# Performance work log

Measured on AMD Instinct MI355X. Metric: run time of the kernel, lower is better.

The kernel has to match this reference:

```python
import jax, jax.numpy as jnp
import numpy as np

NHEAD = 16

def setup_inputs() -> dict:
    key = jax.random.key(0)
    ks = jax.random.split(key, 7)
    b, l, d = 4, 2048, 1024
    s = 1.0 / np.sqrt(d)
    return {
        "Q": jax.random.normal(ks[0], (b, l, d), jnp.float32),
        "K": jax.random.normal(ks[1], (b, l, d), jnp.float32),
        "V": jax.random.normal(ks[2], (b, l, d), jnp.float32),
        "WQ": jax.random.normal(ks[3], (d, d), jnp.float32) * s,
        "WK": jax.random.normal(ks[4], (d, d), jnp.float32) * s,
        "WV": jax.random.normal(ks[5], (d, d), jnp.float32) * s,
        "WO": jax.random.normal(ks[6], (d, d), jnp.float32) * s,
    }

def reference(Q, K, V, WQ, WK, WV, WO):
    # WQ/WK/WV/WO stored torch-style as [out, in]; Linear(x) = x @ W.T
    b, lq, d = Q.shape
    lk = K.shape[1]
    h = NHEAD
    dk = d // h
    # project and split heads: [b, l, h, dk]
    q = (Q @ WQ.T).reshape(b, lq, h, dk)
    k = (K @ WK.T).reshape(b, lk, h, dk)
    v = (V @ WV.T).reshape(b, lk, h, dk)
    # scaled dot-product attention (dropout = identity in eval mode)
    scale = 1.0 / jnp.sqrt(jnp.asarray(dk, Q.dtype))
    score = jnp.einsum('bqhd,bkhd->bhqk', q, k) * scale  # [b,h,lq,lk]
    attn = jax.nn.softmax(score, axis=-1)
    o = jnp.einsum('bhqk,bkhd->bqhd', attn, v).reshape(b, lq, h * dk)
    return o @ WO.T
```

## Files before the change

kernel.cpp:

```cpp
#include <hip/hip_runtime.h>
#include <stdint.h>

#define D_MODEL 1024
#define NHEADS 16
#define DKH 64
#define SEQ 2048
#define BATCH 4
#define M_TOT (BATCH * SEQ)
#define LOG2E 1.44269504088896340736f

typedef __bf16 v8bf __attribute__((ext_vector_type(8)));
typedef __bf16 v4bf __attribute__((ext_vector_type(4)));
typedef _Float16 v4h __attribute__((ext_vector_type(4)));
typedef float v4f __attribute__((ext_vector_type(4)));

typedef const __attribute__((address_space(1))) void* gas_ptr;
typedef __attribute__((address_space(3))) void* las_ptr;

static __device__ __forceinline__ void async16(const void* g, void* l) {
    __builtin_amdgcn_global_load_lds((gas_ptr)g, (las_ptr)l, 16, 0, 0);
}

static __device__ __forceinline__ v4f mfma16x32(v8bf a, v8bf b, v4f c) {
    return __builtin_amdgcn_mfma_f32_16x16x32_bf16(a, b, c, 0, 0, 0);
}
static __device__ __forceinline__ v4f mfma16x16h(v4h a, v4h b, v4f c) {
    return __builtin_amdgcn_mfma_f32_16x16x16f16(a, b, c, 0, 0, 0);
}

__global__ __launch_bounds__(256) void cvt_w(const float* __restrict__ w0,
                                             const float* __restrict__ w1,
                                             const float* __restrict__ w2,
                                             const float* __restrict__ w3,
                                             __bf16* __restrict__ dst) {
    int gid = blockIdx.x * 256 + threadIdx.x;
    int tsel = gid >> 17;
    int off = gid & 131071;
    const float* s = (tsel == 0) ? w0 : (tsel == 1) ? w1 : (tsel == 2) ? w2 : w3;
    const float4* sp = (const float4*)s + 2 * (size_t)off;
    float4 a = sp[0], b = sp[1];
    v8bf o;
    o[0] = (__bf16)a.x; o[1] = (__bf16)a.y; o[2] = (__bf16)a.z; o[3] = (__bf16)a.w;
    o[4] = (__bf16)b.x; o[5] = (__bf16)b.y; o[6] = (__bf16)b.z; o[7] = (__bf16)b.w;
    *(v8bf*)(dst + ((size_t)tsel << 20) + (size_t)off * 8) = o;
}

__global__ __launch_bounds__(256) void gemm_qkv(const float* __restrict__ Q,
                                                const float* __restrict__ K,
                                                const float* __restrict__ V,
                                                const __bf16* __restrict__ Wb,
                                                __bf16* __restrict__ qh,
                                                __bf16* __restrict__ kh,
                                                _Float16* __restrict__ vt) {
    const int t = threadIdx.x, lane = t & 63, wave = t >> 6;
    const int r = lane & 15, qd = lane >> 4;
    const int z = blockIdx.z;
    const int m0 = blockIdx.x * 128, n0 = blockIdx.y * 128;
    const int mw = (wave & 1) * 64, nw = (wave >> 1) * 64;
    const float* A = (z == 0) ? Q : (z == 1) ? K : V;
    const __bf16* W = Wb + ((size_t)z << 20);

    __shared__ __align__(16) __bf16 As[128 * 32];
    __shared__ __align__(16) __bf16 Bs[128 * 32];

    const int arow = t >> 1, ak = (t & 1) * 16;
    const float* ag = A + (size_t)(m0 + arow) * D_MODEL + ak;
    const int aswz = (arow >> 1) & 3;
    const int p0 = ((t & 1) * 2) ^ aswz, p1 = ((t & 1) * 2 + 1) ^ aswz;
    const int wc = (lane & 3) ^ ((lane >> 3) & 3);
    const int wrow = lane >> 2;
    const int rdpos = (qd ^ ((r >> 1) & 3)) * 8;

    v4f acc[4][4] = {};
    for (int k0 = 0; k0 < D_MODEL; k0 += 32) {
#pragma unroll
        for (int p = 0; p < 2; ++p) {
            int rb = (p * 4 + wave) * 16;
            async16(W + (size_t)(n0 + rb + wrow) * D_MODEL + k0 + wc * 8, &Bs[rb * 32]);
        }
        float4 f0 = *(const float4*)(ag + k0);
        float4 f1 = *(const float4*)(ag + k0 + 4);
        float4 f2 = *(const float4*)(ag + k0 + 8);
        float4 f3 = *(const float4*)(ag + k0 + 12);
        v8bf b0, b1;
        b0[0] = (__bf16)f0.x; b0[1] = (__bf16)f0.y; b0[2] = (__bf16)f0.z; b0[3] = (__bf16)f0.w;
        b0[4] = (__bf16)f1.x; b0[5] = (__bf16)f1.y; b0[6] = (__bf16)f1.z; b0[7] = (__bf16)f1.w;
        b1[0] = (__bf16)f2.x; b1[1] = (__bf16)f2.y; b1[2] = (__bf16)f2.z; b1[3] = (__bf16)f2.w;
        b1[4] = (__bf16)f3.x; b1[5] = (__bf16)f3.y; b1[6] = (__bf16)f3.z; b1[7] = (__bf16)f3.w;
        *(v8bf*)&As[arow * 32 + p0 * 8] = b0;
        *(v8bf*)&As[arow * 32 + p1 * 8] = b1;
        __syncthreads();
        v8bf af[4], bfr[4];
#pragma unroll
        for (int mt = 0; mt < 4; ++mt)
            af[mt] = *(const v8bf*)&As[(mw + mt * 16 + r) * 32 + rdpos];
#pragma unroll
        for (int nt = 0; nt < 4; ++nt)
            bfr[nt] = *(const v8bf*)&Bs[(nw + nt * 16 + r) * 32 + rdpos];
#pragma unroll
        for (int mt = 0; mt < 4; ++mt)
#pragma unroll
            for (int nt = 0; nt < 4; ++nt)
                acc[mt][nt] = mfma16x32(af[mt], bfr[nt], acc[mt][nt]);
        __syncthreads();
    }

    const float sc = (z == 0) ? 0.125f * LOG2E : 1.0f;
#pragma unroll
    for (int mt = 0; mt < 4; ++mt)
#pragma unroll
        for (int nt = 0; nt < 4; ++nt) {
            int row = m0 + mw + mt * 16 + qd * 4;
            int col = n0 + nw + nt * 16 + r;
            int bb = row >> 11, l = row & (SEQ - 1);
            int h = col >> 6, d = col & (DKH - 1);
            if (z == 2) {
                v4h o;
#pragma unroll
                for (int i = 0; i < 4; ++i) o[i] = (_Float16)acc[mt][nt][i];
                *(v4h*)&vt[((size_t)((bb * NHEADS + h) * DKH + d)) * SEQ + l] = o;
            } else {
                __bf16* dst = (z == 0) ? qh : kh;
#pragma unroll
                for (int i = 0; i < 4; ++i)
                    dst[(((size_t)(bb * NHEADS + h) * SEQ) + l + i) * DKH + d] =
                        (__bf16)(acc[mt][nt][i] * sc);
            }
        }
}

__global__ __launch_bounds__(256) void gemm_out(const __bf16* __restrict__ A,
                                                const __bf16* __restrict__ W,
                                                float* __restrict__ C) {
    const int t = threadIdx.x, lane = t & 63, wave = t >> 6;
    const int r = lane & 15, qd = lane >> 4;
    const int m0 = blockIdx.x * 128, n0 = blockIdx.y * 128;
    const int mw = (wave & 1) * 64, nw = (wave >> 1) * 64;

    __shared__ __align__(16) __bf16 As[128 * 32];
    __shared__ __align__(16) __bf16 Bs[128 * 32];

    const int wc = (lane & 3) ^ ((lane >> 3) & 3);
    const int wrow = lane >> 2;
    const int rdpos = (qd ^ ((r >> 1) & 3)) * 8;

    v4f acc[4][4] = {};
    for (int k0 = 0; k0 < D_MODEL; k0 += 32) {
#pragma unroll
        for (int p = 0; p < 2; ++p) {
            int rb = (p * 4 + wave) * 16;
            async16(A + (size_t)(m0 + rb + wrow) * D_MODEL + k0 + wc * 8, &As[rb * 32]);
            async16(W + (size_t)(n0 + rb + wrow) * D_MODEL + k0 + wc * 8, &Bs[rb * 32]);
        }
        __syncthreads();
        v8bf af[4], bfr[4];
#pragma unroll
        for (int mt = 0; mt < 4; ++mt)
            af[mt] = *(const v8bf*)&As[(mw + mt * 16 + r) * 32 + rdpos];
#pragma unroll
        for (int nt = 0; nt < 4; ++nt)
            bfr[nt] = *(const v8bf*)&Bs[(nw + nt * 16 + r) * 32 + rdpos];
#pragma unroll
        for (int mt = 0; mt < 4; ++mt)
#pragma unroll
            for (int nt = 0; nt < 4; ++nt)
                acc[mt][nt] = mfma16x32(af[mt], bfr[nt], acc[mt][nt]);
        __syncthreads();
    }
#pragma unroll
    for (int mt = 0; mt < 4; ++mt)
#pragma unroll
        for (int nt = 0; nt < 4; ++nt) {
            int row = m0 + mw + mt * 16 + qd * 4;
            int col = n0 + nw + nt * 16 + r;
#pragma unroll
            for (int i = 0; i < 4; ++i)
                C[(size_t)(row + i) * D_MODEL + col] = acc[mt][nt][i];
        }
}

__global__ __launch_bounds__(256, 4) void attn_kernel(const __bf16* __restrict__ qh,
                                                      const __bf16* __restrict__ kh,
                                                      const _Float16* __restrict__ vt,
                                                      __bf16* __restrict__ oh) {
    const int t = threadIdx.x, lane = t & 63, wave = t >> 6;
    const int r = lane & 15, qd = lane >> 4;
    const int id = blockIdx.x;
    const int bh = (id & 7) * 8 + ((id >> 3) & 7);
    const int qt = id >> 6;
    const int q0 = qt * 128 + wave * 32;

    __shared__ __align__(16) __bf16 Kb[2][64 * 64];
    __shared__ __align__(16) _Float16 Vb[2][64 * 64];

    const __bf16* kbh = kh + (size_t)bh * SEQ * DKH;
    const _Float16* vbh = vt + (size_t)bh * DKH * SEQ;

    v8bf qf[2][2];
#pragma unroll
    for (int a = 0; a < 2; ++a) {
        const __bf16* qp = qh + ((size_t)bh * SEQ + q0 + a * 16 + r) * DKH + qd * 8;
        qf[a][0] = *(const v8bf*)qp;
        qf[a][1] = *(const v8bf*)(qp + 32);
    }

    const int srow = lane >> 3;
    const int schunk = (lane & 7) ^ srow;

#pragma unroll
    for (int p = 0; p < 2; ++p) {
        int rb = wave * 16 + p * 8;
        async16(kbh + (size_t)(rb + srow) * DKH + schunk * 8, &Kb[0][rb * 64]);
        async16(vbh + (size_t)(rb + srow) * SEQ + schunk * 8, &Vb[0][rb * 64]);
    }

    v4f oacc[2][4] = {};
    float lsum[2] = {0.f, 0.f};
    const int rs = r & 7;

    for (int tt = 0; tt < SEQ / 64; ++tt) {
        const int buf = tt & 1;
        __syncthreads();
        if (tt + 1 < SEQ / 64) {
            const int t0 = (tt + 1) * 64;
#pragma unroll
            for (int p = 0; p < 2; ++p) {
                int rb = wave * 16 + p * 8;
                async16(kbh + (size_t)(t0 + rb + srow) * DKH + schunk * 8, &Kb[buf ^ 1][rb * 64]);
                async16(vbh + (size_t)(rb + srow) * SEQ + t0 + schunk * 8, &Vb[buf ^ 1][rb * 64]);
            }
        }
        const __bf16* Kc = Kb[buf];
        const _Float16* Vc = Vb[buf];
#pragma unroll
        for (int kg = 0; kg < 4; ++kg) {
            v8bf kf0 = *(const v8bf*)&Kc[(kg * 16 + r) * 64 + (qd ^ rs) * 8];
            v8bf kf1 = *(const v8bf*)&Kc[(kg * 16 + r) * 64 + ((qd + 4) ^ rs) * 8];
            v4h pf[2];
#pragma unroll
            for (int a = 0; a < 2; ++a) {
                v4f s = mfma16x32(kf0, qf[a][0], v4f{});
                s = mfma16x32(kf1, qf[a][1], s);
                float tsum = 0.f;
#pragma unroll
                for (int i = 0; i < 4; ++i) {
                    float p = __builtin_exp2f(s[i]);
                    pf[a][i] = (_Float16)p;
                    tsum += p;
                }
                lsum[a] += tsum;
            }
#pragma unroll
            for (int g = 0; g < 4; ++g) {
                v4h vf = *(const v4h*)&Vc[(g * 16 + r) * 64 +
                                          ((kg * 2 + (qd >> 1)) ^ rs) * 8 + (qd & 1) * 4];
#pragma unroll
                for (int a = 0; a < 2; ++a)
                    oacc[a][g] = mfma16x16h(vf, pf[a], oacc[a][g]);
            }
        }
    }

    const int b = bh >> 4, h = bh & (NHEADS - 1);
#pragma unroll
    for (int a = 0; a < 2; ++a) {
        float u = lsum[a];
        u += __shfl_xor(u, 16);
        u += __shfl_xor(u, 32);
        float inv = 1.0f / u;
        int l = q0 + a * 16 + r;
        __bf16* op = oh + (((size_t)(b * SEQ + l)) * NHEADS + h) * DKH + qd * 4;
#pragma unroll
        for (int g = 0; g < 4; ++g) {
            v4bf ov;
#pragma unroll
            for (int i = 0; i < 4; ++i) ov[i] = (__bf16)(oacc[a][g][i] * inv);
            *(v4bf*)(op + g * 16) = ov;
        }
    }
}

extern "C" void kernel_launch(void* const* d_in, const int* in_sizes, int n_in,
                              void* d_out, int out_size, void* d_ws, size_t ws_size,
                              hipStream_t stream) {
    const float* Q = (const float*)d_in[0];
    const float* K = (const float*)d_in[1];
    const float* V = (const float*)d_in[2];
    const float* WQ = (const float*)d_in[3];
    const float* WK = (const float*)d_in[4];
    const float* WV = (const float*)d_in[5];
    const float* WO = (const float*)d_in[6];
    float* out = (float*)d_out;

    const size_t elems = (size_t)M_TOT * D_MODEL;
    const size_t welems = (size_t)D_MODEL * D_MODEL;
    __bf16* wb = (__bf16*)d_ws;
    __bf16* qh = wb + 4 * welems;
    __bf16* kh = qh + elems;
    _Float16* vtb = (_Float16*)(kh + elems);
    __bf16* oh = (__bf16*)(vtb + elems);

    cvt_w<<<2048, 256, 0, stream>>>(WQ, WK, WV, WO, wb);
    gemm_qkv<<<dim3(M_TOT / 128, D_MODEL / 128, 3), 256, 0, stream>>>(Q, K, V, wb, qh, kh, vtb);
    attn_kernel<<<1024, 256, 0, stream>>>(qh, kh, vtb, oh);
    gemm_out<<<dim3(M_TOT / 128, D_MODEL / 128), 256, 0, stream>>>(oh, wb + 3 * welems, out);
}
```

Before: 378.6 us.

## Load K/V fragments directly from global into registers, permuting V layout

The attention kernel no longer stages K and V tiles through double-buffered shared memory with async copies and block barriers. Each wave now loads its K and V MFMA fragments straight from global memory into registers, prefetching the next 32-key step. To make the V fragment a contiguous 8-element load, the projection kernel writes V transposed with a permuted sequence order inside each 32-element group. This removes LDS traffic and __syncthreads, but each of the four waves now fetches the same K/V separately, relying on cache. The occupancy hint drops from 4 to 3 blocks to give room for the extra registers.

```diff
diff --git a/kernel.cpp b/kernel.cpp
--- a/kernel.cpp
+++ b/kernel.cpp
@@ -11,6 +11,7 @@
 
 typedef __bf16 v8bf __attribute__((ext_vector_type(8)));
 typedef __bf16 v4bf __attribute__((ext_vector_type(4)));
+typedef _Float16 v8h __attribute__((ext_vector_type(8)));
 typedef _Float16 v4h __attribute__((ext_vector_type(4)));
 typedef float v4f __attribute__((ext_vector_type(4)));
 
@@ -115,10 +116,11 @@
             int bb = row >> 11, l = row & (SEQ - 1);
             int h = col >> 6, d = col & (DKH - 1);
             if (z == 2) {
+                int pos = (l & ~31) + (((l >> 2) & 3) << 3) + (((l >> 4) & 1) << 2);
                 v4h o;
 #pragma unroll
                 for (int i = 0; i < 4; ++i) o[i] = (_Float16)acc[mt][nt][i];
-                *(v4h*)&vt[((size_t)((bb * NHEADS + h) * DKH + d)) * SEQ + l] = o;
+                *(v4h*)&vt[((size_t)((bb * NHEADS + h) * DKH + d)) * SEQ + pos] = o;
             } else {
                 __bf16* dst = (z == 0) ? qh : kh;
 #pragma unroll
@@ -179,19 +181,15 @@
         }
 }
 
-__global__ __launch_bounds__(256, 4) void attn_kernel(const __bf16* __restrict__ qh,
+__global__ __launch_bounds__(256, 3) void attn_kernel(const __bf16* __restrict__ qh,
                                                       const __bf16* __restrict__ kh,
                                                       const _Float16* __restrict__ vt,
                                                       __bf16* __restrict__ oh) {
-    const int t = threadIdx.x, lane = t & 63, wave = t >> 6;
+    const int lane = threadIdx.x & 63, wave = threadIdx.x >> 6;
     const int r = lane & 15, qd = lane >> 4;
     const int id = blockIdx.x;
     const int bh = (id & 7) * 8 + ((id >> 3) & 7);
-    const int qt = id >> 6;
-    const int q0 = qt * 128 + wave * 32;
-
-    __shared__ __align__(16) __bf16 Kb[2][64 * 64];
-    __shared__ __align__(16) _Float16 Vb[2][64 * 64];
+    const int q0 = (id >> 6) * 128 + wave * 32;
 
     const __bf16* kbh = kh + (size_t)bh * SEQ * DKH;
     const _Float16* vbh = vt + (size_t)bh * DKH * SEQ;
@@ -204,61 +202,65 @@
         qf[a][1] = *(const v8bf*)(qp + 32);
     }
 
-    const int srow = lane >> 3;
-    const int schunk = (lane & 7) ^ srow;
-
-#pragma unroll
-    for (int p = 0; p < 2; ++p) {
-        int rb = wave * 16 + p * 8;
-        async16(kbh + (size_t)(rb + srow) * DKH + schunk * 8, &Kb[0][rb * 64]);
-        async16(vbh + (size_t)(rb + srow) * SEQ + schunk * 8, &Vb[0][rb * 64]);
-    }
-
     v4f oacc[2][4] = {};
     float lsum[2] = {0.f, 0.f};
-    const int rs = r & 7;
-
-    for (int tt = 0; tt < SEQ / 64; ++tt) {
-        const int buf = tt & 1;
-        __syncthreads();
-        if (tt + 1 < SEQ / 64) {
-            const int t0 = (tt + 1) * 64;
-#pragma unroll
-            for (int p = 0; p < 2; ++p) {
-                int rb = wave * 16 + p * 8;
-                async16(kbh + (size_t)(t0 + rb + srow) * DKH + schunk * 8, &Kb[buf ^ 1][rb * 64]);
-                async16(vbh + (size_t)(rb + srow) * SEQ + t0 + schunk * 8, &Vb[buf ^ 1][rb * 64]);
-            }
-        }
-        const __bf16* Kc = Kb[buf];
-        const _Float16* Vc = Vb[buf];
-#pragma unroll
-        for (int kg = 0; kg < 4; ++kg) {
-            v8bf kf0 = *(const v8bf*)&Kc[(kg * 16 + r) * 64 + (qd ^ rs) * 8];
-            v8bf kf1 = *(const v8bf*)&Kc[(kg * 16 + r) * 64 + ((qd + 4) ^ rs) * 8];
-            v4h pf[2];
+
+    const __bf16* kp0 = kbh + (size_t)r * DKH + qd * 8;
+    const _Float16* vp0 = vbh + (size_t)r * SEQ + qd * 8;
+
+    v8bf kf[4];
+    v8h vv[4];
+    kf[0] = *(const v8bf*)kp0;
+    kf[1] = *(const v8bf*)(kp0 + 32);
+    kf[2] = *(const v8bf*)(kp0 + 16 * DKH);
+    kf[3] = *(const v8bf*)(kp0 + 16 * DKH + 32);
+#pragma unroll
+    for (int g = 0; g < 4; ++g)
+        vv[g] = *(const v8h*)(vp0 + (size_t)g * 16 * SEQ);
+
+    for (int k0 = 0; k0 < SEQ; k0 += 32) {
+        const int kn = (k0 + 32) & (SEQ - 1);
+        const __bf16* kp = kp0 + (size_t)kn * DKH;
+        const _Float16* vp = vp0 + kn;
+        v8bf kf2[4];
+        v8h vv2[4];
+        kf2[0] = *(const v8bf*)kp;
+        kf2[1] = *(const v8bf*)(kp + 32);
+        kf2[2] = *(const v8bf*)(kp + 16 * DKH);
+        kf2[3] = *(const v8bf*)(kp + 16 * DKH + 32);
+#pragma unroll
+        for (int g = 0; g < 4; ++g)
+            vv2[g] = *(const v8h*)(vp + (size_t)g * 16 * SEQ);
+
+        v4h pf[2][2];
+#pragma unroll
+        for (int kg = 0; kg < 2; ++kg)
 #pragma unroll
             for (int a = 0; a < 2; ++a) {
-                v4f s = mfma16x32(kf0, qf[a][0], v4f{});
-                s = mfma16x32(kf1, qf[a][1], s);
+                v4f s = mfma16x32(kf[kg * 2], qf[a][0], v4f{});
+                s = mfma16x32(kf[kg * 2 + 1], qf[a][1], s);
                 float tsum = 0.f;
 #pragma unroll
                 for (int i = 0; i < 4; ++i) {
                     float p = __builtin_exp2f(s[i]);
-                    pf[a][i] = (_Float16)p;
+                    pf[kg][a][i] = (_Float16)p;
                     tsum += p;
                 }
                 lsum[a] += tsum;
             }
-#pragma unroll
-            for (int g = 0; g < 4; ++g) {
-                v4h vf = *(const v4h*)&Vc[(g * 16 + r) * 64 +
-                                          ((kg * 2 + (qd >> 1)) ^ rs) * 8 + (qd & 1) * 4];
-#pragma unroll
-                for (int a = 0; a < 2; ++a)
-                    oacc[a][g] = mfma16x16h(vf, pf[a], oacc[a][g]);
+
+#pragma unroll
+        for (int g = 0; g < 4; ++g) {
+            v4h vlo = __builtin_shufflevector(vv[g], vv[g], 0, 1, 2, 3);
+            v4h vhi = __builtin_shufflevector(vv[g], vv[g], 4, 5, 6, 7);
+#pragma unroll
+            for (int a = 0; a < 2; ++a) {
+                oacc[a][g] = mfma16x16h(vlo, pf[0][a], oacc[a][g]);
+                oacc[a][g] = mfma16x16h(vhi, pf[1][a], oacc[a][g]);
             }
         }
+#pragma unroll
+        for (int j = 0; j < 4; ++j) { kf[j] = kf2[j]; vv[j] = vv2[j]; }
     }
 
     const int b = bh >> 4, h = bh & (NHEADS - 1);
```

After: 499.5 us. 31.9% more time.

## Pre-convert activations to bf16 and widen attention query tiles with MFMA row sums

Applied to the files above, without the earlier changes.

Activations Q/K/V are first converted to bf16 by a separate kernel, so the QKV projections can reuse the async-LDS bf16 GEMM template instead of loading fp32 and converting inside the inner loop. Each projection now runs as its own launch, and V is written in a permuted column order so attention can read 8 contiguous halves per lane. The attention kernel doubles its query tile to 64 rows per wave, which reuses each K/V tile across more queries. It also computes softmax row sums with an MFMA against a ones vector instead of scalar adds and shuffles. The costs are extra launches, an extra fp32-to-bf16 pass through memory, and higher register pressure in attention, whose launch bound drops from 4 to 2 blocks per CU.

```diff
diff --git a/kernel.cpp b/kernel.cpp
--- a/kernel.cpp
+++ b/kernel.cpp
@@ -11,6 +11,7 @@
 
 typedef __bf16 v8bf __attribute__((ext_vector_type(8)));
 typedef __bf16 v4bf __attribute__((ext_vector_type(4)));
+typedef _Float16 v8h __attribute__((ext_vector_type(8)));
 typedef _Float16 v4h __attribute__((ext_vector_type(4)));
 typedef float v4f __attribute__((ext_vector_type(4)));
 
@@ -26,6 +27,17 @@
 }
 static __device__ __forceinline__ v4f mfma16x16h(v4h a, v4h b, v4f c) {
     return __builtin_amdgcn_mfma_f32_16x16x16f16(a, b, c, 0, 0, 0);
+}
+
+__global__ __launch_bounds__(256) void cvt_x(const float* __restrict__ src,
+                                             __bf16* __restrict__ dst) {
+    int i = blockIdx.x * 256 + threadIdx.x;
+    const float4* s = (const float4*)src;
+    float4 a = s[2 * i], b = s[2 * i + 1];
+    v8bf o;
+    o[0] = (__bf16)a.x; o[1] = (__bf16)a.y; o[2] = (__bf16)a.z; o[3] = (__bf16)a.w;
+    o[4] = (__bf16)b.x; o[5] = (__bf16)b.y; o[6] = (__bf16)b.z; o[7] = (__bf16)b.w;
+    *(v8bf*)(dst + (size_t)i * 8) = o;
 }
 
 __global__ __launch_bounds__(256) void cvt_w(const float* __restrict__ w0,
@@ -45,93 +57,10 @@
     *(v8bf*)(dst + ((size_t)tsel << 20) + (size_t)off * 8) = o;
 }
 
-__global__ __launch_bounds__(256) void gemm_qkv(const float* __restrict__ Q,
-                                                const float* __restrict__ K,
-                                                const float* __restrict__ V,
-                                                const __bf16* __restrict__ Wb,
-                                                __bf16* __restrict__ qh,
-                                                __bf16* __restrict__ kh,
-                                                _Float16* __restrict__ vt) {
-    const int t = threadIdx.x, lane = t & 63, wave = t >> 6;
-    const int r = lane & 15, qd = lane >> 4;
-    const int z = blockIdx.z;
-    const int m0 = blockIdx.x * 128, n0 = blockIdx.y * 128;
-    const int mw = (wave & 1) * 64, nw = (wave >> 1) * 64;
-    const float* A = (z == 0) ? Q : (z == 1) ? K : V;
-    const __bf16* W = Wb + ((size_t)z << 20);
-
-    __shared__ __align__(16) __bf16 As[128 * 32];
-    __shared__ __align__(16) __bf16 Bs[128 * 32];
-
-    const int arow = t >> 1, ak = (t & 1) * 16;
-    const float* ag = A + (size_t)(m0 + arow) * D_MODEL + ak;
-    const int aswz = (arow >> 1) & 3;
-    const int p0 = ((t & 1) * 2) ^ aswz, p1 = ((t & 1) * 2 + 1) ^ aswz;
-    const int wc = (lane & 3) ^ ((lane >> 3) & 3);
-    const int wrow = lane >> 2;
-    const int rdpos = (qd ^ ((r >> 1) & 3)) * 8;
-
-    v4f acc[4][4] = {};
-    for (int k0 = 0; k0 < D_MODEL; k0 += 32) {
-#pragma unroll
-        for (int p = 0; p < 2; ++p) {
-            int rb = (p * 4 + wave) * 16;
-            async16(W + (size_t)(n0 + rb + wrow) * D_MODEL + k0 + wc * 8, &Bs[rb * 32]);
-        }
-        float4 f0 = *(const float4*)(ag + k0);
-        float4 f1 = *(const float4*)(ag + k0 + 4);
-        float4 f2 = *(const float4*)(ag + k0 + 8);
-        float4 f3 = *(const float4*)(ag + k0 + 12);
-        v8bf b0, b1;
-        b0[0] = (__bf16)f0.x; b0[1] = (__bf16)f0.y; b0[2] = (__bf16)f0.z; b0[3] = (__bf16)f0.w;
-        b0[4] = (__bf16)f1.x; b0[5] = (__bf16)f1.y; b0[6] = (__bf16)f1.z; b0[7] = (__bf16)f1.w;
-        b1[0] = (__bf16)f2.x; b1[1] = (__bf16)f2.y; b1[2] = (__bf16)f2.z; b1[3] = (__bf16)f2.w;
-        b1[4] = (__bf16)f3.x; b1[5] = (__bf16)f3.y; b1[6] = (__bf16)f3.z; b1[7] = (__bf16)f3.w;
-        *(v8bf*)&As[arow * 32 + p0 * 8] = b0;
-        *(v8bf*)&As[arow * 32 + p1 * 8] = b1;
-        __syncthreads();
-        v8bf af[4], bfr[4];
-#pragma unroll
-        for (int mt = 0; mt < 4; ++mt)
-            af[mt] = *(const v8bf*)&As[(mw + mt * 16 + r) * 32 + rdpos];
-#pragma unroll
-        for (int nt = 0; nt < 4; ++nt)
-            bfr[nt] = *(const v8bf*)&Bs[(nw + nt * 16 + r) * 32 + rdpos];
-#pragma unroll
-        for (int mt = 0; mt < 4; ++mt)
-#pragma unroll
-            for (int nt = 0; nt < 4; ++nt)
-                acc[mt][nt] = mfma16x32(af[mt], bfr[nt], acc[mt][nt]);
-        __syncthreads();
-    }
-
-    const float sc = (z == 0) ? 0.125f * LOG2E : 1.0f;
-#pragma unroll
-    for (int mt = 0; mt < 4; ++mt)
-#pragma unroll
-        for (int nt = 0; nt < 4; ++nt) {
-            int row = m0 + mw + mt * 16 + qd * 4;
-            int col = n0 + nw + nt * 16 + r;
-            int bb = row >> 11, l = row & (SEQ - 1);
-            int h = col >> 6, d = col & (DKH - 1);
-            if (z == 2) {
-                v4h o;
-#pragma unroll
-                for (int i = 0; i < 4; ++i) o[i] = (_Float16)acc[mt][nt][i];
-                *(v4h*)&vt[((size_t)((bb * NHEADS + h) * DKH + d)) * SEQ + l] = o;
-            } else {
-                __bf16* dst = (z == 0) ? qh : kh;
-#pragma unroll
-                for (int i = 0; i < 4; ++i)
-                    dst[(((size_t)(bb * NHEADS + h) * SEQ) + l + i) * DKH + d] =
-                        (__bf16)(acc[mt][nt][i] * sc);
-            }
-        }
-}
-
-__global__ __launch_bounds__(256) void gemm_out(const __bf16* __restrict__ A,
-                                                const __bf16* __restrict__ W,
-                                                float* __restrict__ C) {
+template <int LAYOUT>
+__global__ __launch_bounds__(256) void gemm_nt(const __bf16* __restrict__ A,
+                                               const __bf16* __restrict__ W,
+                                               void* __restrict__ Cv, float scale) {
     const int t = threadIdx.x, lane = t & 63, wave = t >> 6;
     const int r = lane & 15, qd = lane >> 4;
     const int m0 = blockIdx.x * 128, n0 = blockIdx.y * 128;
@@ -167,28 +96,48 @@
                 acc[mt][nt] = mfma16x32(af[mt], bfr[nt], acc[mt][nt]);
         __syncthreads();
     }
+
 #pragma unroll
     for (int mt = 0; mt < 4; ++mt)
 #pragma unroll
         for (int nt = 0; nt < 4; ++nt) {
             int row = m0 + mw + mt * 16 + qd * 4;
             int col = n0 + nw + nt * 16 + r;
-#pragma unroll
-            for (int i = 0; i < 4; ++i)
-                C[(size_t)(row + i) * D_MODEL + col] = acc[mt][nt][i];
-        }
-}
-
-__global__ __launch_bounds__(256, 4) void attn_kernel(const __bf16* __restrict__ qh,
+            if (LAYOUT == 0) {
+                float* C = (float*)Cv;
+#pragma unroll
+                for (int i = 0; i < 4; ++i)
+                    C[(size_t)(row + i) * D_MODEL + col] = acc[mt][nt][i];
+            } else {
+                int bb = row >> 11, l = row & (SEQ - 1);
+                int h = col >> 6, d = col & (DKH - 1);
+                if (LAYOUT == 2) {
+                    int pos = (l & ~31) + (((l >> 2) & 3) << 3) + (((l >> 4) & 1) << 2);
+                    _Float16* vt = (_Float16*)Cv;
+                    v4h o;
+#pragma unroll
+                    for (int i = 0; i < 4; ++i) o[i] = (_Float16)acc[mt][nt][i];
+                    *(v4h*)&vt[((size_t)((bb * NHEADS + h) * DKH + d)) * SEQ + pos] = o;
+                } else {
+                    __bf16* dst = (__bf16*)Cv;
+#pragma unroll
+                    for (int i = 0; i < 4; ++i)
+                        dst[(((size_t)(bb * NHEADS + h) * SEQ) + l + i) * DKH + d] =
+                            (__bf16)(acc[mt][nt][i] * scale);
+                }
+            }
+        }
+}
+
+__global__ __launch_bounds__(256, 2) void attn_kernel(const __bf16* __restrict__ qh,
                                                       const __bf16* __restrict__ kh,
                                                       const _Float16* __restrict__ vt,
                                                       __bf16* __restrict__ oh) {
-    const int t = threadIdx.x, lane = t & 63, wave = t >> 6;
+    const int lane = threadIdx.x & 63, wave = threadIdx.x >> 6;
     const int r = lane & 15, qd = lane >> 4;
     const int id = blockIdx.x;
     const int bh = (id & 7) * 8 + ((id >> 3) & 7);
-    const int qt = id >> 6;
-    const int q0 = qt * 128 + wave * 32;
+    const int q0 = (id >> 6) * 256 + wave * 64;
 
     __shared__ __align__(16) __bf16 Kb[2][64 * 64];
     __shared__ __align__(16) _Float16 Vb[2][64 * 64];
@@ -196,27 +145,30 @@
     const __bf16* kbh = kh + (size_t)bh * SEQ * DKH;
     const _Float16* vbh = vt + (size_t)bh * DKH * SEQ;
 
-    v8bf qf[2][2];
-#pragma unroll
-    for (int a = 0; a < 2; ++a) {
+    v8bf qf[4][2];
+#pragma unroll
+    for (int a = 0; a < 4; ++a) {
         const __bf16* qp = qh + ((size_t)bh * SEQ + q0 + a * 16 + r) * DKH + qd * 8;
         qf[a][0] = *(const v8bf*)qp;
         qf[a][1] = *(const v8bf*)(qp + 32);
     }
 
+    v4f oacc[4][4] = {};
+    v4f psum[4] = {};
+    v4h ones;
+    ones[0] = (_Float16)1.f; ones[1] = (_Float16)1.f;
+    ones[2] = (_Float16)1.f; ones[3] = (_Float16)1.f;
+
     const int srow = lane >> 3;
-    const int schunk = (lane & 7) ^ srow;
+    const int sc = (lane & 7) ^ srow;
+    const int rs = r & 7;
 
 #pragma unroll
     for (int p = 0; p < 2; ++p) {
         int rb = wave * 16 + p * 8;
-        async16(kbh + (size_t)(rb + srow) * DKH + schunk * 8, &Kb[0][rb * 64]);
-        async16(vbh + (size_t)(rb + srow) * SEQ + schunk * 8, &Vb[0][rb * 64]);
-    }
-
-    v4f oacc[2][4] = {};
-    float lsum[2] = {0.f, 0.f};
-    const int rs = r & 7;
+        async16(kbh + (size_t)(rb + srow) * DKH + sc * 8, &Kb[0][rb * 64]);
+        async16(vbh + (size_t)(rb + srow) * SEQ + sc * 8, &Vb[0][rb * 64]);
+    }
 
     for (int tt = 0; tt < SEQ / 64; ++tt) {
         const int buf = tt & 1;
@@ -226,48 +178,52 @@
 #pragma unroll
             for (int p = 0; p < 2; ++p) {
                 int rb = wave * 16 + p * 8;
-                async16(kbh + (size_t)(t0 + rb + srow) * DKH + schunk * 8, &Kb[buf ^ 1][rb * 64]);
-                async16(vbh + (size_t)(rb + srow) * SEQ + t0 + schunk * 8, &Vb[buf ^ 1][rb * 64]);
+                async16(kbh + (size_t)(t0 + rb + srow) * DKH + sc * 8, &Kb[buf ^ 1][rb * 64]);
+                async16(vbh + (size_t)(rb + srow) * SEQ + t0 + sc * 8, &Vb[buf ^ 1][rb * 64]);
             }
         }
         const __bf16* Kc = Kb[buf];
         const _Float16* Vc = Vb[buf];
 #pragma unroll
-        for (int kg = 0; kg < 4; ++kg) {
-            v8bf kf0 = *(const v8bf*)&Kc[(kg * 16 + r) * 64 + (qd ^ rs) * 8];
-            v8bf kf1 = *(const v8bf*)&Kc[(kg * 16 + r) * 64 + ((qd + 4) ^ rs) * 8];
-            v4h pf[2];
-#pragma unroll
-            for (int a = 0; a < 2; ++a) {
-                v4f s = mfma16x32(kf0, qf[a][0], v4f{});
-                s = mfma16x32(kf1, qf[a][1], s);
-                float tsum = 0.f;
-#pragma unroll
-                for (int i = 0; i < 4; ++i) {
-                    float p = __builtin_exp2f(s[i]);
-                    pf[a][i] = (_Float16)p;
-                    tsum += p;
+        for (int kb = 0; kb < 2; ++kb) {
+            v4h pf[2][4];
+#pragma unroll
+            for (int kg = 0; kg < 2; ++kg) {
+                int row = kb * 32 + kg * 16 + r;
+                v8bf ka = *(const v8bf*)&Kc[row * 64 + (qd ^ rs) * 8];
+                v8bf kc = *(const v8bf*)&Kc[row * 64 + ((qd + 4) ^ rs) * 8];
+#pragma unroll
+                for (int a = 0; a < 4; ++a) {
+                    v4f s = mfma16x32(ka, qf[a][0], v4f{});
+                    s = mfma16x32(kc, qf[a][1], s);
+#pragma unroll
+                    for (int i = 0; i < 4; ++i)
+                        pf[kg][a][i] = (_Float16)__builtin_exp2f(s[i]);
                 }
-                lsum[a] += tsum;
+            }
+#pragma unroll
+            for (int a = 0; a < 4; ++a) {
+                psum[a] = mfma16x16h(ones, pf[0][a], psum[a]);
+                psum[a] = mfma16x16h(ones, pf[1][a], psum[a]);
             }
 #pragma unroll
             for (int g = 0; g < 4; ++g) {
-                v4h vf = *(const v4h*)&Vc[(g * 16 + r) * 64 +
-                                          ((kg * 2 + (qd >> 1)) ^ rs) * 8 + (qd & 1) * 4];
-#pragma unroll
-                for (int a = 0; a < 2; ++a)
-                    oacc[a][g] = mfma16x16h(vf, pf[a], oacc[a][g]);
+                v8h vv = *(const v8h*)&Vc[(g * 16 + r) * 64 + ((kb * 4 + qd) ^ rs) * 8];
+                v4h vlo = __builtin_shufflevector(vv, vv, 0, 1, 2, 3);
+                v4h vhi = __builtin_shufflevector(vv, vv, 4, 5, 6, 7);
+#pragma unroll
+                for (int a = 0; a < 4; ++a) {
+                    oacc[a][g] = mfma16x16h(vlo, pf[0][a], oacc[a][g]);
+                    oacc[a][g] = mfma16x16h(vhi, pf[1][a], oacc[a][g]);
+                }
             }
         }
     }
 
     const int b = bh >> 4, h = bh & (NHEADS - 1);
 #pragma unroll
-    for (int a = 0; a < 2; ++a) {
-        float u = lsum[a];
-        u += __shfl_xor(u, 16);
-        u += __shfl_xor(u, 32);
-        float inv = 1.0f / u;
+    for (int a = 0; a < 4; ++a) {
+        float inv = 1.0f / psum[a][0];
         int l = q0 + a * 16 + r;
         __bf16* op = oh + (((size_t)(b * SEQ + l)) * NHEADS + h) * DKH + qd * 4;
 #pragma unroll
@@ -295,13 +251,21 @@
     const size_t elems = (size_t)M_TOT * D_MODEL;
     const size_t welems = (size_t)D_MODEL * D_MODEL;
     __bf16* wb = (__bf16*)d_ws;
-    __bf16* qh = wb + 4 * welems;
+    __bf16* xb = wb + 4 * welems;
+    __bf16* qh = xb + elems;
     __bf16* kh = qh + elems;
     _Float16* vtb = (_Float16*)(kh + elems);
     __bf16* oh = (__bf16*)(vtb + elems);
 
+    dim3 gg(M_TOT / 128, D_MODEL / 128);
+
     cvt_w<<<2048, 256, 0, stream>>>(WQ, WK, WV, WO, wb);
-    gemm_qkv<<<dim3(M_TOT / 128, D_MODEL / 128, 3), 256, 0, stream>>>(Q, K, V, wb, qh, kh, vtb);
-    attn_kernel<<<1024, 256, 0, stream>>>(qh, kh, vtb, oh);
-    gemm_out<<<dim3(M_TOT / 128, D_MODEL / 128), 256, 0, stream>>>(oh, wb + 3 * welems, out);
-}
+    cvt_x<<<4096, 256, 0, stream>>>(Q, xb);
+    gemm_nt<1><<<gg, 256, 0, stream>>>(xb, wb, qh, 0.125f * LOG2E);
+    cvt_x<<<4096, 256, 0, stream>>>(K, xb);
+    gemm_nt<1><<<gg, 256, 0, stream>>>(xb, wb + welems, kh, 1.0f);
+    cvt_x<<<4096, 256, 0, stream>>>(V, xb);
+    gemm_nt<2><<<gg, 256, 0, stream>>>(xb, wb + 2 * welems, vtb, 1.0f);
+    attn_kernel<<<512, 256, 0, stream>>>(qh, kh, vtb, oh);
+    gemm_nt<0><<<gg, 256, 0, stream>>>(oh, wb + 3 * welems, out, 1.0f);
+}
```

New measurement: 377.4 us. About the same (-0.3%).
